# Kernel tuning notes

Measured on AMD Instinct MI355X. Metric: run time of the kernel, lower is better.

## Reference

```python
import jax, jax.numpy as jnp
import numpy as np

N_NODES = 150000
N_EDGES = 2400000
F_IN = 128
HID = 32
N_CLS = 1


def setup_inputs() -> dict:
    key = jax.random.key(0)
    ks = jax.random.split(key, 8)
    x = jax.random.normal(ks[0], (N_NODES, F_IN), dtype=jnp.float32)
    edge_index = jax.random.randint(ks[1], (2, N_EDGES), 0, N_NODES, dtype=jnp.int64)
    # Glorot-ish scaled weights
    W1 = jax.random.normal(ks[2], (F_IN, HID), dtype=jnp.float32) * (1.0 / np.sqrt(F_IN))
    b1 = jnp.zeros((HID,), dtype=jnp.float32)
    W2 = jax.random.normal(ks[3], (HID, HID), dtype=jnp.float32) * (1.0 / np.sqrt(HID))
    b2 = jnp.zeros((HID,), dtype=jnp.float32)
    W3 = jax.random.normal(ks[4], (HID, N_CLS), dtype=jnp.float32) * (1.0 / np.sqrt(HID))
    b3 = jnp.zeros((N_CLS,), dtype=jnp.float32)
    return {"x": x, "edge_index": edge_index, "W1": W1, "b1": b1,
            "W2": W2, "b2": b2, "W3": W3, "b3": b3}


def reference(x, edge_index, W1, b1, W2, b2, W3, b3):
    # GCNConv (Kipf & Welling): add self-loops, symmetric normalization,
    # transform-then-aggregate. Dropout omitted (inference: training=False).
    n = x.shape[0]
    loop = jnp.arange(n, dtype=edge_index.dtype)
    src = jnp.concatenate([edge_index[0], loop])  # [E+N]
    dst = jnp.concatenate([edge_index[1], loop])  # [E+N]
    deg = jax.ops.segment_sum(jnp.ones(src.shape[0], x.dtype), dst, num_segments=n)
    deg_inv_sqrt = jax.lax.rsqrt(jnp.maximum(deg, 1.0))  # deg >= 1 (self-loops)
    norm = (deg_inv_sqrt[src] * deg_inv_sqrt[dst])[:, None]  # [E+N, 1]

    def gcn_conv(h, W, b):
        h = h @ W                                   # [N, out]
        msg = h[src] * norm                         # gather + scale  [E+N, out]
        return jax.ops.segment_sum(msg, dst, num_segments=n) + b

    h = jax.nn.relu(gcn_conv(x, W1, b1))
    h = jax.nn.relu(gcn_conv(h, W2, b2))
    return jax.nn.sigmoid(gcn_conv(h, W3, b3))      # [N, 1]
```

## Files before the change

kernel.cpp:

```cpp
#include <hip/hip_runtime.h>
#include <math.h>

#define F_IN 128
#define HID  32

#define NPB   256
#define MAXNB 1024
#define EPB   8192
#define BLK_E 1024
#define BLK_C 512

#define XPAD  132

__device__ __forceinline__ void fma4(float4& a, float s, const float4& w) {
    a.x = fmaf(s, w.x, a.x);
    a.y = fmaf(s, w.y, a.y);
    a.z = fmaf(s, w.z, a.z);
    a.w = fmaf(s, w.w, a.w);
}

__device__ __forceinline__ void add4(float4& a, const float4& v) {
    a.x += v.x; a.y += v.y; a.z += v.z; a.w += v.w;
}


__global__ __launch_bounds__(BLK_E) void k_bhist(const int* __restrict__ dst,
                                                 int* __restrict__ bin_hist,
                                                 int e, int nbuckets) {
    __shared__ int h[MAXNB];
    int tid = threadIdx.x;
    for (int i = tid; i < nbuckets; i += BLK_E) h[i] = 0;
    __syncthreads();
    int base = blockIdx.x * EPB;
    if (base + EPB <= e) {
        const int4* d4 = (const int4*)(dst + base);
#pragma unroll
        for (int i = tid; i < EPB / 4; i += BLK_E) {
            int4 v = d4[i];
            atomicAdd(&h[v.x >> 8], 1);
            atomicAdd(&h[v.y >> 8], 1);
            atomicAdd(&h[v.z >> 8], 1);
            atomicAdd(&h[v.w >> 8], 1);
        }
    } else {
        int end = e;
        for (int i = base + tid; i < end; i += BLK_E)
            atomicAdd(&h[dst[i] >> 8], 1);
    }
    __syncthreads();
    for (int i = tid; i < nbuckets; i += BLK_E)
        if (h[i]) atomicAdd(&bin_hist[i], h[i]);
}

__global__ __launch_bounds__(1024) void k_bscan(const int* __restrict__ bin_hist,
                                                int* __restrict__ bin_off,
                                                int* __restrict__ bin_cur,
                                                int* __restrict__ offsets,
                                                int nbuckets, int n, int e) {
    __shared__ int sh[MAXNB];
    int t = threadIdx.x;
    int v = (t < nbuckets) ? bin_hist[t] : 0;
    sh[t] = v; __syncthreads();
    for (int off = 1; off < MAXNB; off <<= 1) {
        int a = (t >= off) ? sh[t - off] : 0;
        __syncthreads();
        sh[t] += a;
        __syncthreads();
    }
    int excl = sh[t] - v;
    if (t < nbuckets) { bin_off[t] = excl; bin_cur[t] = excl; }
    if (t == 0) { bin_off[nbuckets] = e; offsets[n] = e; }
}

__global__ __launch_bounds__(BLK_E) void k_bpart(const int* __restrict__ src,
                                                 const int* __restrict__ dst,
                                                 int* __restrict__ bin_cur,
                                                 unsigned* __restrict__ tmp,
                                                 int e, int nbuckets) {
    __shared__ int h[MAXNB];
    __shared__ int lc[MAXNB];
    int tid = threadIdx.x;
    for (int i = tid; i < nbuckets; i += BLK_E) h[i] = 0;
    __syncthreads();
    int base = blockIdx.x * EPB;
    bool full = (base + EPB <= e);
    if (full) {
        const int4* d4 = (const int4*)(dst + base);
#pragma unroll
        for (int i = tid; i < EPB / 4; i += BLK_E) {
            int4 v = d4[i];
            atomicAdd(&h[v.x >> 8], 1);
            atomicAdd(&h[v.y >> 8], 1);
            atomicAdd(&h[v.z >> 8], 1);
            atomicAdd(&h[v.w >> 8], 1);
        }
    } else {
        for (int i = base + tid; i < e; i += BLK_E)
            atomicAdd(&h[dst[i] >> 8], 1);
    }
    __syncthreads();
    for (int i = tid; i < nbuckets; i += BLK_E) {
        int c = h[i];
        h[i] = c ? atomicAdd(&bin_cur[i], c) : 0;
        lc[i] = 0;
    }
    __syncthreads();
    if (full) {
        const int4* s4 = (const int4*)(src + base);
        const int4* d4 = (const int4*)(dst + base);
#pragma unroll
        for (int i = tid; i < EPB / 4; i += BLK_E) {
            int4 sv = s4[i];
            int4 dv = d4[i];
            int b0 = dv.x >> 8; int r0 = atomicAdd(&lc[b0], 1);
            tmp[h[b0] + r0] = (unsigned)sv.x | ((unsigned)(dv.x & (NPB - 1)) << 18);
            int b1 = dv.y >> 8; int r1 = atomicAdd(&lc[b1], 1);
            tmp[h[b1] + r1] = (unsigned)sv.y | ((unsigned)(dv.y & (NPB - 1)) << 18);
            int b2 = dv.z >> 8; int r2 = atomicAdd(&lc[b2], 1);
            tmp[h[b2] + r2] = (unsigned)sv.z | ((unsigned)(dv.z & (NPB - 1)) << 18);
            int b3 = dv.w >> 8; int r3 = atomicAdd(&lc[b3], 1);
            tmp[h[b3] + r3] = (unsigned)sv.w | ((unsigned)(dv.w & (NPB - 1)) << 18);
        }
    } else {
        for (int i = base + tid; i < e; i += BLK_E) {
            int d = dst[i];
            int b = d >> 8;
            int r = atomicAdd(&lc[b], 1);
            tmp[h[b] + r] = (unsigned)src[i] | ((unsigned)(d & (NPB - 1)) << 18);
        }
    }
}

__global__ __launch_bounds__(BLK_C) void k_bcsr(const unsigned* __restrict__ tmp,
                                                const int* __restrict__ bin_off,
                                                int* __restrict__ es,
                                                int* __restrict__ offsets,
                                                float* __restrict__ dis, int n) {
    __shared__ int cnt[NPB];
    __shared__ int sh[NPB];
    __shared__ int cur[NPB];
    int b = blockIdx.x, t = threadIdx.x;
    if (t < NPB) cnt[t] = 0;
    __syncthreads();
    int s0 = bin_off[b], s1 = bin_off[b + 1];
    for (int i = s0 + t; i < s1; i += BLK_C)
        atomicAdd(&cnt[(tmp[i] >> 18) & (NPB - 1)], 1);
    __syncthreads();
    int v = (t < NPB) ? cnt[t] : 0;
    if (t < NPB) sh[t] = v;
    __syncthreads();
    for (int off = 1; off < NPB; off <<= 1) {
        int a = (t < NPB && t >= off) ? sh[t - off] : 0;
        __syncthreads();
        if (t < NPB) sh[t] += a;
        __syncthreads();
    }
    if (t < NPB) {
        int excl = sh[t] - v;
        int node = b * NPB + t;
        if (node < n) {
            offsets[node] = s0 + excl;
            dis[node] = rsqrtf((float)(v + 1));
        }
        cur[t] = excl;
    }
    __syncthreads();
    for (int i = s0 + t; i < s1; i += BLK_C) {
        unsigned w = tmp[i];
        int dl = (w >> 18) & (NPB - 1);
        int r = atomicAdd(&cur[dl], 1);
        es[s0 + r] = (int)(w & 0x3FFFFu);
    }
}


__global__ __launch_bounds__(256) void k_gemm1(const float* __restrict__ x,
                                               const float* __restrict__ W,
                                               const float* __restrict__ dis,
                                               float* __restrict__ u, int n) {
    __shared__ float Ws[F_IN * HID];
    __shared__ float Xs[64 * XPAD];
    int tid = threadIdx.x;
    for (int i = tid; i < F_IN * HID; i += 256) Ws[i] = W[i];
    int node0 = blockIdx.x * 64;
#pragma unroll
    for (int it = 0; it < 8; ++it) {
        int c  = it * 256 + tid;
        int r  = c >> 5;
        int c4 = c & 31;
        int gr = node0 + r;
        if (gr >= n) gr = n - 1;
        float4 v = *(const float4*)&x[(size_t)gr * F_IN + c4 * 4];
        *(float4*)&Xs[r * XPAD + c4 * 4] = v;
    }
    int cg = tid & 7, gq = tid >> 3;
    float4 acc[2];
    acc[0] = make_float4(0.f, 0.f, 0.f, 0.f);
    acc[1] = make_float4(0.f, 0.f, 0.f, 0.f);
    __syncthreads();
#pragma unroll 4
    for (int ks = 0; ks < 32; ++ks) {
        float4 xv[2];
        xv[0] = *(const float4*)&Xs[gq * XPAD + ks * 4];
        xv[1] = *(const float4*)&Xs[(gq + 32) * XPAD + ks * 4];
        float4 w0 = *(const float4*)&Ws[(ks * 4 + 0) * HID + cg * 4];
        float4 w1 = *(const float4*)&Ws[(ks * 4 + 1) * HID + cg * 4];
        float4 w2 = *(const float4*)&Ws[(ks * 4 + 2) * HID + cg * 4];
        float4 w3 = *(const float4*)&Ws[(ks * 4 + 3) * HID + cg * 4];
#pragma unroll
        for (int m = 0; m < 2; ++m) {
            fma4(acc[m], xv[m].x, w0);
            fma4(acc[m], xv[m].y, w1);
            fma4(acc[m], xv[m].z, w2);
            fma4(acc[m], xv[m].w, w3);
        }
    }
#pragma unroll
    for (int m = 0; m < 2; ++m) {
        int node = node0 + gq + 32 * m;
        if (node < n) {
            float ds = dis[node];
            float4 r;
            r.x = acc[m].x * ds; r.y = acc[m].y * ds;
            r.z = acc[m].z * ds; r.w = acc[m].w * ds;
            *(float4*)&u[(size_t)node * HID + cg * 4] = r;
        }
    }
}

__global__ __launch_bounds__(256) void k_gemm2(const float* __restrict__ h,
                                               const float* __restrict__ W,
                                               const float* __restrict__ dis,
                                               float* __restrict__ u, int n) {
    __shared__ float Ws[HID * HID];
    int tid = threadIdx.x;
    for (int i = tid; i < HID * HID; i += 256) Ws[i] = W[i];
    int node0 = blockIdx.x * 64;
    int cg = tid & 7, gq = tid >> 3;
    int row[2];
#pragma unroll
    for (int m = 0; m < 2; ++m) {
        int node = node0 + gq + 32 * m;
        row[m] = (node < n) ? node : 0;
    }
    const float4* h4 = (const float4*)h;
    float4 acc[2];
#pragma unroll
    for (int m = 0; m < 2; ++m) acc[m] = make_float4(0.f, 0.f, 0.f, 0.f);
    __syncthreads();
#pragma unroll 4
    for (int ks = 0; ks < 8; ++ks) {
        float4 xv[2];
#pragma unroll
        for (int m = 0; m < 2; ++m) xv[m] = h4[(size_t)row[m] * 8 + ks];
        float4 w0 = *(const float4*)&Ws[(ks * 4 + 0) * HID + cg * 4];
        float4 w1 = *(const float4*)&Ws[(ks * 4 + 1) * HID + cg * 4];
        float4 w2 = *(const float4*)&Ws[(ks * 4 + 2) * HID + cg * 4];
        float4 w3 = *(const float4*)&Ws[(ks * 4 + 3) * HID + cg * 4];
#pragma unroll
        for (int m = 0; m < 2; ++m) {
            fma4(acc[m], xv[m].x, w0);
            fma4(acc[m], xv[m].y, w1);
            fma4(acc[m], xv[m].z, w2);
            fma4(acc[m], xv[m].w, w3);
        }
    }
#pragma unroll
    for (int m = 0; m < 2; ++m) {
        int node = node0 + gq + 32 * m;
        if (node < n) {
            float ds = dis[node];
            float4 r;
            r.x = acc[m].x * ds; r.y = acc[m].y * ds;
            r.z = acc[m].z * ds; r.w = acc[m].w * ds;
            *(float4*)&u[(size_t)node * HID + cg * 4] = r;
        }
    }
}


__global__ __launch_bounds__(256) void k_gather32(const float4* __restrict__ u4,
                                                  const int* __restrict__ es,
                                                  const int* __restrict__ offsets,
                                                  const float* __restrict__ dis,
                                                  const float* __restrict__ b,
                                                  float4* __restrict__ h4, int n) {
    int t = blockIdx.x * 256 + threadIdx.x;
    int node = t >> 3, q = t & 7;
    if (node >= n) return;
    int s0 = offsets[node];
    int s1 = offsets[node + 1];
    float4 acc = u4[(size_t)node * 8 + q];
    int ei = s0;
    for (; ei + 8 <= s1; ei += 8) {
        int e0 = es[ei], e1 = es[ei + 1], e2 = es[ei + 2], e3 = es[ei + 3];
        int e4 = es[ei + 4], e5 = es[ei + 5], e6 = es[ei + 6], e7 = es[ei + 7];
        float4 v0 = u4[(size_t)e0 * 8 + q];
        float4 v1 = u4[(size_t)e1 * 8 + q];
        float4 v2 = u4[(size_t)e2 * 8 + q];
        float4 v3 = u4[(size_t)e3 * 8 + q];
        float4 v4 = u4[(size_t)e4 * 8 + q];
        float4 v5 = u4[(size_t)e5 * 8 + q];
        float4 v6 = u4[(size_t)e6 * 8 + q];
        float4 v7 = u4[(size_t)e7 * 8 + q];
        acc.x += ((v0.x + v1.x) + (v2.x + v3.x)) + ((v4.x + v5.x) + (v6.x + v7.x));
        acc.y += ((v0.y + v1.y) + (v2.y + v3.y)) + ((v4.y + v5.y) + (v6.y + v7.y));
        acc.z += ((v0.z + v1.z) + (v2.z + v3.z)) + ((v4.z + v5.z) + (v6.z + v7.z));
        acc.w += ((v0.w + v1.w) + (v2.w + v3.w)) + ((v4.w + v5.w) + (v6.w + v7.w));
    }
    for (; ei + 4 <= s1; ei += 4) {
        int e0 = es[ei], e1 = es[ei + 1], e2 = es[ei + 2], e3 = es[ei + 3];
        float4 v0 = u4[(size_t)e0 * 8 + q];
        float4 v1 = u4[(size_t)e1 * 8 + q];
        float4 v2 = u4[(size_t)e2 * 8 + q];
        float4 v3 = u4[(size_t)e3 * 8 + q];
        acc.x += (v0.x + v1.x) + (v2.x + v3.x);
        acc.y += (v0.y + v1.y) + (v2.y + v3.y);
        acc.z += (v0.z + v1.z) + (v2.z + v3.z);
        acc.w += (v0.w + v1.w) + (v2.w + v3.w);
    }
    for (; ei < s1; ++ei) {
        int s = es[ei];
        float4 v = u4[(size_t)s * 8 + q];
        add4(acc, v);
    }
    float ds = dis[node];
    float4 r;
    r.x = fmaxf(fmaf(ds, acc.x, b[q * 4 + 0]), 0.0f);
    r.y = fmaxf(fmaf(ds, acc.y, b[q * 4 + 1]), 0.0f);
    r.z = fmaxf(fmaf(ds, acc.z, b[q * 4 + 2]), 0.0f);
    r.w = fmaxf(fmaf(ds, acc.w, b[q * 4 + 3]), 0.0f);
    h4[(size_t)node * 8 + q] = r;
}

__global__ __launch_bounds__(256) void k_gather32_dot(const float4* __restrict__ u4,
                                                      const int* __restrict__ es,
                                                      const int* __restrict__ offsets,
                                                      const float* __restrict__ dis,
                                                      const float* __restrict__ b,
                                                      const float* __restrict__ W3,
                                                      float* __restrict__ s, int n) {
    int t = blockIdx.x * 256 + threadIdx.x;
    int node = t >> 3, q = t & 7;
    if (node >= n) return;
    int s0 = offsets[node];
    int s1 = offsets[node + 1];
    float4 acc = u4[(size_t)node * 8 + q];
    int ei = s0;
    for (; ei + 8 <= s1; ei += 8) {
        int e0 = es[ei], e1 = es[ei + 1], e2 = es[ei + 2], e3 = es[ei + 3];
        int e4 = es[ei + 4], e5 = es[ei + 5], e6 = es[ei + 6], e7 = es[ei + 7];
        float4 v0 = u4[(size_t)e0 * 8 + q];
        float4 v1 = u4[(size_t)e1 * 8 + q];
        float4 v2 = u4[(size_t)e2 * 8 + q];
        float4 v3 = u4[(size_t)e3 * 8 + q];
        float4 v4 = u4[(size_t)e4 * 8 + q];
        float4 v5 = u4[(size_t)e5 * 8 + q];
        float4 v6 = u4[(size_t)e6 * 8 + q];
        float4 v7 = u4[(size_t)e7 * 8 + q];
        acc.x += ((v0.x + v1.x) + (v2.x + v3.x)) + ((v4.x + v5.x) + (v6.x + v7.x));
        acc.y += ((v0.y + v1.y) + (v2.y + v3.y)) + ((v4.y + v5.y) + (v6.y + v7.y));
        acc.z += ((v0.z + v1.z) + (v2.z + v3.z)) + ((v4.z + v5.z) + (v6.z + v7.z));
        acc.w += ((v0.w + v1.w) + (v2.w + v3.w)) + ((v4.w + v5.w) + (v6.w + v7.w));
    }
    for (; ei + 4 <= s1; ei += 4) {
        int e0 = es[ei], e1 = es[ei + 1], e2 = es[ei + 2], e3 = es[ei + 3];
        float4 v0 = u4[(size_t)e0 * 8 + q];
        float4 v1 = u4[(size_t)e1 * 8 + q];
        float4 v2 = u4[(size_t)e2 * 8 + q];
        float4 v3 = u4[(size_t)e3 * 8 + q];
        acc.x += (v0.x + v1.x) + (v2.x + v3.x);
        acc.y += (v0.y + v1.y) + (v2.y + v3.y);
        acc.z += (v0.z + v1.z) + (v2.z + v3.z);
        acc.w += (v0.w + v1.w) + (v2.w + v3.w);
    }
    for (; ei < s1; ++ei) {
        int sc = es[ei];
        float4 v = u4[(size_t)sc * 8 + q];
        add4(acc, v);
    }
    float ds = dis[node];
    float4 r;
    r.x = fmaxf(fmaf(ds, acc.x, b[q * 4 + 0]), 0.0f);
    r.y = fmaxf(fmaf(ds, acc.y, b[q * 4 + 1]), 0.0f);
    r.z = fmaxf(fmaf(ds, acc.z, b[q * 4 + 2]), 0.0f);
    r.w = fmaxf(fmaf(ds, acc.w, b[q * 4 + 3]), 0.0f);
    float p = r.x * W3[q * 4 + 0] + r.y * W3[q * 4 + 1]
            + r.z * W3[q * 4 + 2] + r.w * W3[q * 4 + 3];
    p += __shfl_down(p, 4, 8);
    p += __shfl_down(p, 2, 8);
    p += __shfl_down(p, 1, 8);
    if (q == 0) s[node] = p * ds;
}

__global__ void k_gather1(const float* __restrict__ sv, const int* __restrict__ es,
                          const int* __restrict__ offsets, const float* __restrict__ dis,
                          const float* __restrict__ b3, float* __restrict__ out, int n) {
    int d = blockIdx.x * 256 + threadIdx.x;
    if (d >= n) return;
    float acc = sv[d];
    int s0 = offsets[d], s1 = offsets[d + 1];
    int ei = s0;
    for (; ei + 4 <= s1; ei += 4) {
        float v0 = sv[es[ei]], v1 = sv[es[ei + 1]];
        float v2 = sv[es[ei + 2]], v3 = sv[es[ei + 3]];
        acc += (v0 + v1) + (v2 + v3);
    }
    for (; ei < s1; ++ei) acc += sv[es[ei]];
    float z = dis[d] * acc + b3[0];
    out[d] = 1.0f / (1.0f + expf(-z));
}


extern "C" void kernel_launch(void* const* d_in, const int* in_sizes, int n_in,
                              void* d_out, int out_size, void* d_ws, size_t ws_size,
                              hipStream_t stream) {
    const float* x  = (const float*)d_in[0];
    const int*   ei = (const int*)d_in[1];
    const float* W1 = (const float*)d_in[2];
    const float* b1 = (const float*)d_in[3];
    const float* W2 = (const float*)d_in[4];
    const float* b2 = (const float*)d_in[5];
    const float* W3 = (const float*)d_in[6];
    const float* b3 = (const float*)d_in[7];
    float* out = (float*)d_out;

    int n = out_size;
    int e = in_sizes[1] / 2;
    const int* src = ei;
    const int* dst = ei + e;

    int nbuckets = (n + NPB - 1) / NPB;

    float* A        = (float*)d_ws;
    float* B        = A + (size_t)n * HID;
    float* dis      = B + (size_t)n * HID;
    float* Cs       = dis + n;
    int*   offsets  = (int*)(Cs + n);
    int*   es       = offsets + (n + 1);
    int*   bin_hist = es + e;
    int*   bin_off  = bin_hist + nbuckets;
    int*   bin_cur  = bin_off + (nbuckets + 1);
    unsigned* tmp   = (unsigned*)B;

    dim3 blk(256);
    int gN    = (n + 255) / 256;
    int gN8   = (n * 8 + 255) / 256;
    int g64   = (n + 63) / 64;
    int gEb   = (e + EPB - 1) / EPB;

    hipMemsetAsync(bin_hist, 0, (size_t)nbuckets * sizeof(int), stream);
    k_bhist<<<gEb, dim3(BLK_E), 0, stream>>>(dst, bin_hist, e, nbuckets);
    k_bscan<<<1, 1024, 0, stream>>>(bin_hist, bin_off, bin_cur, offsets, nbuckets, n, e);
    k_bpart<<<gEb, dim3(BLK_E), 0, stream>>>(src, dst, bin_cur, tmp, e, nbuckets);
    k_bcsr <<<nbuckets, dim3(BLK_C), 0, stream>>>(tmp, bin_off, es, offsets, dis, n);

    k_gemm1   <<<g64, blk, 0, stream>>>(x, W1, dis, A, n);
    k_gather32<<<gN8, blk, 0, stream>>>((const float4*)A, es, offsets, dis, b1, (float4*)B, n);

    k_gemm2       <<<g64, blk, 0, stream>>>(B, W2, dis, A, n);
    k_gather32_dot<<<gN8, blk, 0, stream>>>((const float4*)A, es, offsets, dis, b2, W3, Cs, n);

    k_gather1<<<gN, blk, 0, stream>>>(Cs, es, offsets, dis, b3, out, n);
}
```

Before: 323.5 us.

## Fuse layer-2 GEMM into layer-1 gather and reuse per-block bucket histograms

The layer-1 aggregation kernel now also applies W2 to each node's hidden vector. The 8 lanes holding a node exchange their float4 slices via xor shuffles, then each lane computes 4 output columns from W2 kept in shared memory. This removes the separate k_gemm2 launch and one write and re-read of the N×32 hidden buffer. Separately, k_bhist now stores each block's bucket histogram in the workspace so k_bpart can skip re-reading dst to rebuild it, at the cost of extra workspace writes and reads.

```diff
diff --git a/kernel.cpp b/kernel.cpp
--- a/kernel.cpp
+++ b/kernel.cpp
@@ -23,9 +23,19 @@
     a.x += v.x; a.y += v.y; a.z += v.z; a.w += v.w;
 }
 
+__device__ __forceinline__ float4 shx4(float4 v, int m) {
+    float4 r;
+    r.x = __shfl_xor(v.x, m);
+    r.y = __shfl_xor(v.y, m);
+    r.z = __shfl_xor(v.z, m);
+    r.w = __shfl_xor(v.w, m);
+    return r;
+}
+
 
 __global__ __launch_bounds__(BLK_E) void k_bhist(const int* __restrict__ dst,
                                                  int* __restrict__ bin_hist,
+                                                 int* __restrict__ hb,
                                                  int e, int nbuckets) {
     __shared__ int h[MAXNB];
     int tid = threadIdx.x;
@@ -48,8 +58,12 @@
             atomicAdd(&h[dst[i] >> 8], 1);
     }
     __syncthreads();
-    for (int i = tid; i < nbuckets; i += BLK_E)
-        if (h[i]) atomicAdd(&bin_hist[i], h[i]);
+    size_t hbase = (size_t)blockIdx.x * nbuckets;
+    for (int i = tid; i < nbuckets; i += BLK_E) {
+        int c = h[i];
+        if (c) atomicAdd(&bin_hist[i], c);
+        hb[hbase + i] = c;
+    }
 }
 
 __global__ __launch_bounds__(1024) void k_bscan(const int* __restrict__ bin_hist,
@@ -76,35 +90,20 @@
                                                  const int* __restrict__ dst,
                                                  int* __restrict__ bin_cur,
                                                  unsigned* __restrict__ tmp,
+                                                 const int* __restrict__ hb,
                                                  int e, int nbuckets) {
     __shared__ int h[MAXNB];
     __shared__ int lc[MAXNB];
     int tid = threadIdx.x;
-    for (int i = tid; i < nbuckets; i += BLK_E) h[i] = 0;
+    size_t hbase = (size_t)blockIdx.x * nbuckets;
+    for (int i = tid; i < nbuckets; i += BLK_E) {
+        int c = hb[hbase + i];
+        h[i] = c ? atomicAdd(&bin_cur[i], c) : 0;
+        lc[i] = 0;
+    }
     __syncthreads();
     int base = blockIdx.x * EPB;
     bool full = (base + EPB <= e);
-    if (full) {
-        const int4* d4 = (const int4*)(dst + base);
-#pragma unroll
-        for (int i = tid; i < EPB / 4; i += BLK_E) {
-            int4 v = d4[i];
-            atomicAdd(&h[v.x >> 8], 1);
-            atomicAdd(&h[v.y >> 8], 1);
-            atomicAdd(&h[v.z >> 8], 1);
-            atomicAdd(&h[v.w >> 8], 1);
-        }
-    } else {
-        for (int i = base + tid; i < e; i += BLK_E)
-            atomicAdd(&h[dst[i] >> 8], 1);
-    }
-    __syncthreads();
-    for (int i = tid; i < nbuckets; i += BLK_E) {
-        int c = h[i];
-        h[i] = c ? atomicAdd(&bin_cur[i], c) : 0;
-        lc[i] = 0;
-    }
-    __syncthreads();
     if (full) {
         const int4* s4 = (const int4*)(src + base);
         const int4* d4 = (const int4*)(dst + base);
@@ -228,64 +227,19 @@
     }
 }
 
-__global__ __launch_bounds__(256) void k_gemm2(const float* __restrict__ h,
-                                               const float* __restrict__ W,
-                                               const float* __restrict__ dis,
-                                               float* __restrict__ u, int n) {
+
+__global__ __launch_bounds__(256) void k_gather32_g2(const float4* __restrict__ u4,
+                                                     const int* __restrict__ es,
+                                                     const int* __restrict__ offsets,
+                                                     const float* __restrict__ dis,
+                                                     const float* __restrict__ b,
+                                                     const float* __restrict__ W2,
+                                                     float* __restrict__ u2, int n) {
     __shared__ float Ws[HID * HID];
     int tid = threadIdx.x;
-    for (int i = tid; i < HID * HID; i += 256) Ws[i] = W[i];
-    int node0 = blockIdx.x * 64;
-    int cg = tid & 7, gq = tid >> 3;
-    int row[2];
-#pragma unroll
-    for (int m = 0; m < 2; ++m) {
-        int node = node0 + gq + 32 * m;
-        row[m] = (node < n) ? node : 0;
-    }
-    const float4* h4 = (const float4*)h;
-    float4 acc[2];
-#pragma unroll
-    for (int m = 0; m < 2; ++m) acc[m] = make_float4(0.f, 0.f, 0.f, 0.f);
-    __syncthreads();
-#pragma unroll 4
-    for (int ks = 0; ks < 8; ++ks) {
-        float4 xv[2];
-#pragma unroll
-        for (int m = 0; m < 2; ++m) xv[m] = h4[(size_t)row[m] * 8 + ks];
-        float4 w0 = *(const float4*)&Ws[(ks * 4 + 0) * HID + cg * 4];
-        float4 w1 = *(const float4*)&Ws[(ks * 4 + 1) * HID + cg * 4];
-        float4 w2 = *(const float4*)&Ws[(ks * 4 + 2) * HID + cg * 4];
-        float4 w3 = *(const float4*)&Ws[(ks * 4 + 3) * HID + cg * 4];
-#pragma unroll
-        for (int m = 0; m < 2; ++m) {
-            fma4(acc[m], xv[m].x, w0);
-            fma4(acc[m], xv[m].y, w1);
-            fma4(acc[m], xv[m].z, w2);
-            fma4(acc[m], xv[m].w, w3);
-        }
-    }
-#pragma unroll
-    for (int m = 0; m < 2; ++m) {
-        int node = node0 + gq + 32 * m;
-        if (node < n) {
-            float ds = dis[node];
-            float4 r;
-            r.x = acc[m].x * ds; r.y = acc[m].y * ds;
-            r.z = acc[m].z * ds; r.w = acc[m].w * ds;
-            *(float4*)&u[(size_t)node * HID + cg * 4] = r;
-        }
-    }
-}
-
-
-__global__ __launch_bounds__(256) void k_gather32(const float4* __restrict__ u4,
-                                                  const int* __restrict__ es,
-                                                  const int* __restrict__ offsets,
-                                                  const float* __restrict__ dis,
-                                                  const float* __restrict__ b,
-                                                  float4* __restrict__ h4, int n) {
-    int t = blockIdx.x * 256 + threadIdx.x;
+    for (int i = tid; i < HID * HID; i += 256) Ws[i] = W2[i];
+    __syncthreads();
+    int t = blockIdx.x * 256 + tid;
     int node = t >> 3, q = t & 7;
     if (node >= n) return;
     int s0 = offsets[node];
@@ -330,7 +284,44 @@
     r.y = fmaxf(fmaf(ds, acc.y, b[q * 4 + 1]), 0.0f);
     r.z = fmaxf(fmaf(ds, acc.z, b[q * 4 + 2]), 0.0f);
     r.w = fmaxf(fmaf(ds, acc.w, b[q * 4 + 3]), 0.0f);
-    h4[(size_t)node * 8 + q] = r;
+
+    float4 o1 = shx4(r, 1);
+    float4 L0 = (q & 1) ? o1 : r;
+    float4 L1 = (q & 1) ? r  : o1;
+    float4 M0 = shx4(L0, 2);
+    float4 M1 = shx4(L1, 2);
+    float4 P0 = (q & 2) ? M0 : L0;
+    float4 P1 = (q & 2) ? M1 : L1;
+    float4 P2 = (q & 2) ? L0 : M0;
+    float4 P3 = (q & 2) ? L1 : M1;
+    float4 Q0 = shx4(P0, 4);
+    float4 Q1 = shx4(P1, 4);
+    float4 Q2 = shx4(P2, 4);
+    float4 Q3 = shx4(P3, 4);
+    float4 H0 = (q & 4) ? Q0 : P0;
+    float4 H1 = (q & 4) ? Q1 : P1;
+    float4 H2 = (q & 4) ? Q2 : P2;
+    float4 H3 = (q & 4) ? Q3 : P3;
+    float4 H4 = (q & 4) ? P0 : Q0;
+    float4 H5 = (q & 4) ? P1 : Q1;
+    float4 H6 = (q & 4) ? P2 : Q2;
+    float4 H7 = (q & 4) ? P3 : Q3;
+
+    float4 oacc = make_float4(0.f, 0.f, 0.f, 0.f);
+#define G2_STEP(Hj, j) { \
+    float4 w0 = *(const float4*)&Ws[((j) * 4 + 0) * HID + q * 4]; \
+    float4 w1 = *(const float4*)&Ws[((j) * 4 + 1) * HID + q * 4]; \
+    float4 w2 = *(const float4*)&Ws[((j) * 4 + 2) * HID + q * 4]; \
+    float4 w3 = *(const float4*)&Ws[((j) * 4 + 3) * HID + q * 4]; \
+    fma4(oacc, Hj.x, w0); fma4(oacc, Hj.y, w1); \
+    fma4(oacc, Hj.z, w2); fma4(oacc, Hj.w, w3); }
+    G2_STEP(H0, 0) G2_STEP(H1, 1) G2_STEP(H2, 2) G2_STEP(H3, 3)
+    G2_STEP(H4, 4) G2_STEP(H5, 5) G2_STEP(H6, 6) G2_STEP(H7, 7)
+#undef G2_STEP
+    float4 w;
+    w.x = oacc.x * ds; w.y = oacc.y * ds;
+    w.z = oacc.z * ds; w.w = oacc.w * ds;
+    *(float4*)&u2[(size_t)node * HID + q * 4] = w;
 }
 
 __global__ __launch_bounds__(256) void k_gather32_dot(const float4* __restrict__ u4,
@@ -431,6 +422,7 @@
     const int* dst = ei + e;
 
     int nbuckets = (n + NPB - 1) / NPB;
+    int gEb      = (e + EPB - 1) / EPB;
 
     float* A        = (float*)d_ws;
     float* B        = A + (size_t)n * HID;
@@ -441,25 +433,24 @@
     int*   bin_hist = es + e;
     int*   bin_off  = bin_hist + nbuckets;
     int*   bin_cur  = bin_off + (nbuckets + 1);
+    int*   hb       = bin_cur + nbuckets;
     unsigned* tmp   = (unsigned*)B;
 
     dim3 blk(256);
     int gN    = (n + 255) / 256;
     int gN8   = (n * 8 + 255) / 256;
     int g64   = (n + 63) / 64;
-    int gEb   = (e + EPB - 1) / EPB;
 
     hipMemsetAsync(bin_hist, 0, (size_t)nbuckets * sizeof(int), stream);
-    k_bhist<<<gEb, dim3(BLK_E), 0, stream>>>(dst, bin_hist, e, nbuckets);
+    k_bhist<<<gEb, dim3(BLK_E), 0, stream>>>(dst, bin_hist, hb, e, nbuckets);
     k_bscan<<<1, 1024, 0, stream>>>(bin_hist, bin_off, bin_cur, offsets, nbuckets, n, e);
-    k_bpart<<<gEb, dim3(BLK_E), 0, stream>>>(src, dst, bin_cur, tmp, e, nbuckets);
+    k_bpart<<<gEb, dim3(BLK_E), 0, stream>>>(src, dst, bin_cur, tmp, hb, e, nbuckets);
     k_bcsr <<<nbuckets, dim3(BLK_C), 0, stream>>>(tmp, bin_off, es, offsets, dis, n);
 
-    k_gemm1   <<<g64, blk, 0, stream>>>(x, W1, dis, A, n);
-    k_gather32<<<gN8, blk, 0, stream>>>((const float4*)A, es, offsets, dis, b1, (float4*)B, n);
-
-    k_gemm2       <<<g64, blk, 0, stream>>>(B, W2, dis, A, n);
-    k_gather32_dot<<<gN8, blk, 0, stream>>>((const float4*)A, es, offsets, dis, b2, W3, Cs, n);
+    k_gemm1      <<<g64, blk, 0, stream>>>(x, W1, dis, A, n);
+    k_gather32_g2<<<gN8, blk, 0, stream>>>((const float4*)A, es, offsets, dis, b1, W2, B, n);
+
+    k_gather32_dot<<<gN8, blk, 0, stream>>>((const float4*)B, es, offsets, dis, b2, W3, Cs, n);
 
     k_gather1<<<gN, blk, 0, stream>>>(Cs, es, offsets, dis, b3, out, n);
 }
```

Measured after the change: 315.3 us. -2.5%, faster.
